# Performance work log

Measured on AMD Instinct MI355X. Metric: run time of the kernel, lower is better.

Reference implementation:

```python
import jax, jax.numpy as jnp
import numpy as np

TREE_DEPTH = 6
TEMPERATURE = 1.0


def setup_inputs() -> dict:
    key = jax.random.key(0)
    k1, k2, k3, k4, k5 = jax.random.split(key, 5)
    B, D = 8192, 512
    T = 64                      # n_trees
    N = 2 ** TREE_DEPTH - 1    # internal nodes = 63
    L = 2 ** TREE_DEPTH        # leaves = 64
    C = 100                    # classes
    return {
        "x": jax.random.normal(k1, (B, D), dtype=jnp.float32),
        "split_weights": jax.random.normal(k2, (T, N, D), dtype=jnp.float32),
        "split_bias": jax.random.normal(k3, (T, N), dtype=jnp.float32),
        "leaf_logits": jax.random.normal(k4, (T, L, C), dtype=jnp.float32),
        "tree_weights": jax.random.uniform(k5, (T,), dtype=jnp.float32),
    }


def reference(x, split_weights, split_bias, leaf_logits, tree_weights):
    # All node decisions for all trees in one batched GEMM: [B, T, N]
    dec = jax.nn.sigmoid(
        (jnp.einsum("bd,tnd->btn", x, split_weights) + split_bias) / TEMPERATURE
    )
    B = x.shape[0]
    T = split_weights.shape[0]
    L = leaf_logits.shape[1]  # 2 ** TREE_DEPTH
    leaf_ids = jnp.arange(L)
    # Cumulative product of routing probs along each leaf's root-to-leaf path.
    leaf_probs = jnp.ones((B, T, L), dtype=x.dtype)
    for d in range(TREE_DEPTH):
        # ancestor node (level order) of each leaf at this depth
        node_idx = (2 ** d - 1) + (leaf_ids >> (TREE_DEPTH - d))
        # 1 -> right child (prob = dec), 0 -> left child (prob = 1 - dec)
        bit = (leaf_ids >> (TREE_DEPTH - d - 1)) & 1
        dd = dec[:, :, node_idx]  # [B, T, L]
        leaf_probs = leaf_probs * jnp.where(bit.astype(bool), dd, 1.0 - dd)
    tree_out = jax.nn.softmax(leaf_logits, axis=-1)  # [T, L, C]
    # weighted sum over trees of (leaf_probs @ leaf class dists)
    return jnp.einsum("btl,tlc,t->bc", leaf_probs, tree_out, tree_weights)
```

## Files before the change

### kernel.cpp

```cpp
#include <hip/hip_runtime.h>

#define TREES 64
#define NN 63
#define LL 64
#define CC 100
#define CPAD 112
#define DD 512
#define BB 8192

typedef __attribute__((ext_vector_type(8))) _Float16 f16x8;
typedef __attribute__((ext_vector_type(4))) _Float16 f16x4;
typedef __attribute__((ext_vector_type(4))) float floatx4;

#define XH_WS   0
#define SWH_WS  8388608
#define W2T_WS  12582912

__device__ __forceinline__ void gl_lds16(const _Float16* g, char* lds) {
    __builtin_amdgcn_global_load_lds(
        (const __attribute__((address_space(1))) unsigned int*)g,
        (__attribute__((address_space(3))) unsigned int*)lds, 16, 0, 0);
}

__device__ __forceinline__ f16x8 cvt8(const float* s) {
    float4 a = *(const float4*)s, b = *(const float4*)(s + 4);
    f16x8 h;
    h[0]=(_Float16)a.x; h[1]=(_Float16)a.y; h[2]=(_Float16)a.z; h[3]=(_Float16)a.w;
    h[4]=(_Float16)b.x; h[5]=(_Float16)b.y; h[6]=(_Float16)b.z; h[7]=(_Float16)b.w;
    return h;
}

__device__ __forceinline__ float fsig(float x) {
    return __builtin_amdgcn_rcpf(1.f + __expf(-x));
}

__global__ __launch_bounds__(256) void prep_kernel(
    const float* __restrict__ x, const float* __restrict__ sw,
    const float* __restrict__ leaf_logits, const float* __restrict__ tree_w,
    _Float16* __restrict__ xh, _Float16* __restrict__ swh,
    _Float16* __restrict__ w2T, float* __restrict__ out)
{
    if (blockIdx.x < 3072) {
        int i = blockIdx.x * 256 + threadIdx.x;
        if (i < 524288) {
            int tile = i >> 10, cidx = i & 1023;
            int row = cidx >> 3, c = cidx & 7;
            int rb = tile >> 3, kt = tile & 7;
            int gk = kt * 64 + ((c ^ (row & 7)) << 3);
            *(f16x8*)(xh + (size_t)i * 8) = cvt8(x + (size_t)(rb * 128 + row) * DD + gk);
        } else {
            int j = i - 524288;
            if (j < 262144) {
                int tile = j >> 10, cidx = j & 1023;
                int col = cidx >> 3, c = cidx & 7;
                int cb = tile >> 3, kt = tile & 7;
                int tt = col >> 6, node = col & 63;
                f16x8 h = (f16x8)(_Float16)0.f;
                if (node < NN) {
                    int gk = kt * 64 + ((c ^ (col & 7)) << 3);
                    h = cvt8(sw + (size_t)((cb * 2 + tt) * NN + node) * DD + gk);
                }
                *(f16x8*)(swh + (size_t)j * 8) = h;
            }
        }
    } else if (blockIdx.x < 4096) {
        int row  = (blockIdx.x - 3072) * 4 + (threadIdx.x >> 6);
        int lane = threadIdx.x & 63;
        int t = row >> 6, l = row & 63;
        const float* src = leaf_logits + (size_t)row * CC;
        float v0 = (lane < CC)      ? src[lane]      : -1e30f;
        float v1 = (lane + 64 < CC) ? src[lane + 64] : -1e30f;
        float m = fmaxf(v0, v1);
#pragma unroll
        for (int off = 32; off > 0; off >>= 1)
            m = fmaxf(m, __shfl_down(m, off, 64));
        m = __shfl(m, 0, 64);
        float e0 = (lane < CC)      ? __expf(v0 - m) : 0.f;
        float e1 = (lane + 64 < CC) ? __expf(v1 - m) : 0.f;
        float s = e0 + e1;
#pragma unroll
        for (int off = 32; off > 0; off >>= 1)
            s += __shfl_down(s, off, 64);
        s = __shfl(s, 0, 64);
        float scale = tree_w[t] / s;
        _Float16* base = w2T + (size_t)t * CPAD * LL;
#define LSWZ(c) ((((l >> 3) ^ ((c) & 7)) << 3) | (l & 7))
        if (lane < CC)      base[(size_t)lane * LL + LSWZ(lane)]               = (_Float16)(e0 * scale);
        if (lane + 64 < CC) base[(size_t)(lane + 64) * LL + LSWZ(lane + 64)]   = (_Float16)(e1 * scale);
        if (lane < CPAD - CC) base[(size_t)(CC + lane) * LL + LSWZ(CC + lane)] = (_Float16)0.f;
#undef LSWZ
    } else {
        int i = (blockIdx.x - 4096) * 1024 + threadIdx.x * 4;
        *(float4*)(out + i) = make_float4(0.f, 0.f, 0.f, 0.f);
    }
}

#define SETB 24576
#define A_SMEM 49152
__global__ __launch_bounds__(256, 3) void fused_kernel(
    const _Float16* __restrict__ xh,
    const _Float16* __restrict__ swh,
    const float* __restrict__ sb,
    const _Float16* __restrict__ w2T,
    float* __restrict__ out)
{
    __shared__ __align__(16) char smem[A_SMEM];
    _Float16* dec = (_Float16*)smem;
    _Float16* lpl = (_Float16*)(smem + SETB);

    const int tid  = threadIdx.x;
    const int lane = tid & 63;
    const int wid  = tid >> 6;
    const int quad = lane >> 4;
    const int l15  = lane & 15;
    const int rb   = blockIdx.x;
    const int tc   = blockIdx.y;
    const int rb2  = rb >> 1;
    const int half = rb & 1;

    floatx4 oacc2[7];
#pragma unroll
    for (int ni = 0; ni < 7; ++ni) oacc2[ni] = (floatx4)0.f;

    const _Float16* xtile = xh + (size_t)rb2 * 65536 + (size_t)half * 4096;

#define STAGE(WT, KT, SOFF)                                                    \
    {                                                                          \
        _Pragma("unroll")                                                      \
        for (int j = 0; j < 2; ++j)                                            \
            gl_lds16(xtile + (KT) * 8192 + j * 2048 + wid * 512 + lane * 8,    \
                     smem + (SOFF) + j * 4096 + wid * 1024);                   \
        _Pragma("unroll")                                                      \
        for (int j = 0; j < 4; ++j)                                            \
            gl_lds16((WT) + (KT) * 8192 + j * 2048 + wid * 512 + lane * 8,     \
                     smem + (SOFF) + 8192 + j * 4096 + wid * 1024);            \
    }

    STAGE(swh + (size_t)(tc * 4) * 65536, 0, 0);
    __syncthreads();

    for (int tg = 0; tg < 4; ++tg) {
        const int cb = tc * 4 + tg;
        const _Float16* wtile = swh + (size_t)cb * 65536;

        float bias_v[2];
        {
            int mytree = cb * 2 + (wid >> 1);
#pragma unroll
            for (int ni = 0; ni < 2; ++ni) {
                int nd = 32 * (wid & 1) + 16 * ni + l15;
                bias_v[ni] = (nd < NN) ? sb[mytree * NN + nd] : 0.f;
            }
        }

        floatx4 acc[4][2];
#pragma unroll
        for (int i = 0; i < 4; ++i)
#pragma unroll
            for (int j = 0; j < 2; ++j) acc[i][j] = (floatx4)0.f;

        for (int kt = 0; kt < 8; ++kt) {
            if (kt < 7)
                STAGE(wtile, kt + 1, ((kt + 1) & 1) * SETB);
            const int cur = (kt & 1) * SETB;
            const _Float16* xs = (const _Float16*)(smem + cur);
            const _Float16* wl = (const _Float16*)(smem + cur + 8192);
#pragma unroll
            for (int ks = 0; ks < 2; ++ks) {
                f16x8 af[4], bf[2];
#pragma unroll
                for (int mi = 0; mi < 4; ++mi) {
                    int r = 16 * mi + l15;
                    af[mi] = *(const f16x8*)&xs[r * 64 + ((((ks << 2) | quad) ^ (r & 7)) << 3)];
                }
#pragma unroll
                for (int ni = 0; ni < 2; ++ni) {
                    int r = 32 * wid + 16 * ni + l15;
                    bf[ni] = *(const f16x8*)&wl[r * 64 + ((((ks << 2) | quad) ^ (r & 7)) << 3)];
                }
#pragma unroll
                for (int mi = 0; mi < 4; ++mi)
#pragma unroll
                    for (int ni = 0; ni < 2; ++ni)
                        acc[mi][ni] = __builtin_amdgcn_mfma_f32_16x16x32_f16(
                            af[mi], bf[ni], acc[mi][ni], 0, 0, 0);
            }
            __syncthreads();
        }

#pragma unroll
        for (int mi = 0; mi < 4; ++mi) {
            int r0 = 16 * mi + 4 * quad;
#pragma unroll
            for (int ni = 0; ni < 2; ++ni) {
                int col = 32 * wid + 16 * ni + l15;
                f16x4 v;
#pragma unroll
                for (int r = 0; r < 4; ++r)
                    v[r] = (_Float16)(acc[mi][ni][r] + bias_v[ni]);
                *(f16x4*)&dec[col * 66 + r0] = v;
            }
        }
        __syncthreads();

        const int u    = tid >> 7;
        const int tt   = (tid >> 6) & 1;
        const int lrow = tid & 63;
        const int tb   = tt * 64;
        f16x8 lpreg[4];
        {
#define SIG(n) fsig((float)dec[(tb + (n)) * 66 + lrow])
            float d0 = SIG(0);
            float p1 = u ? d0 : 1.f - d0;
            float d1 = SIG(1 + u);
#pragma unroll
            for (int b8 = 0; b8 < 4; ++b8) {
                int i4 = b8 >> 1, i3 = b8 & 1;
                float p2 = p1 * (i4 ? d1 : 1.f - d1);
                float d2 = SIG(3 + 2 * u + i4);
                float p3 = p2 * (i3 ? d2 : 1.f - d2);
                float d3 = SIG(7 + 4 * u + b8);
                f16x8 blk;
#pragma unroll
                for (int i2 = 0; i2 < 2; ++i2) {
                    float p4 = p3 * (i2 ? d3 : 1.f - d3);
                    float d4 = SIG(15 + 8 * u + 2 * b8 + i2);
#pragma unroll
                    for (int i1 = 0; i1 < 2; ++i1) {
                        float p5 = p4 * (i1 ? d4 : 1.f - d4);
                        float d5 = SIG(31 + 16 * u + 4 * b8 + 2 * i2 + i1);
                        blk[i2 * 4 + i1 * 2 + 0] = (_Float16)(p5 * (1.f - d5));
                        blk[i2 * 4 + i1 * 2 + 1] = (_Float16)(p5 * d5);
                    }
                }
                lpreg[b8] = blk;
            }
#undef SIG
        }
#pragma unroll
        for (int b8 = 0; b8 < 4; ++b8) {
            int q = u * 4 + b8;
            *(f16x8*)&lpl[tt * 4096 + lrow * 64 + ((q ^ (lrow & 7)) << 3)] = lpreg[b8];
        }
        __syncthreads();

        if (tg < 3)
            STAGE(swh + (size_t)(cb + 1) * 65536, 0, 0);

        {
            const int tree0 = cb * 2;
            const int rbase = wid * 16;
#pragma unroll
            for (int t = 0; t < 2; ++t) {
                const _Float16* bp = w2T + (size_t)(tree0 + t) * (CPAD * LL) + (size_t)l15 * 64;
                const _Float16* lplt = lpl + t * 4096;
#pragma unroll
                for (int ks = 0; ks < 2; ++ks) {
                    const int sw = (((ks << 2) | quad) ^ (l15 & 7)) << 3;
                    f16x8 bbv[7], abv;
#pragma unroll
                    for (int ni = 0; ni < 7; ++ni)
                        bbv[ni] = *(const f16x8*)(bp + ni * 16 * 64 + sw);
                    abv = *(const f16x8*)&lplt[(rbase + l15) * 64 + sw];
#pragma unroll
                    for (int ni = 0; ni < 7; ++ni)
                        oacc2[ni] = __builtin_amdgcn_mfma_f32_16x16x32_f16(
                            abv, bbv[ni], oacc2[ni], 0, 0, 0);
                }
            }
        }
        __syncthreads();
    }
#undef STAGE

    {
        const int rbase2 = rb * 64 + wid * 16 + 4 * quad;
#pragma unroll
        for (int ni = 0; ni < 7; ++ni) {
            int col = 16 * ni + l15;
            if (col < CC) {
#pragma unroll
                for (int r = 0; r < 4; ++r)
                    unsafeAtomicAdd(&out[(size_t)(rbase2 + r) * CC + col],
                                    oacc2[ni][r]);
            }
        }
    }
}

extern "C" void kernel_launch(void* const* d_in, const int* in_sizes, int n_in,
                              void* d_out, int out_size, void* d_ws, size_t ws_size,
                              hipStream_t stream) {
    const float* x  = (const float*)d_in[0];
    const float* sw = (const float*)d_in[1];
    const float* sb = (const float*)d_in[2];
    const float* ll = (const float*)d_in[3];
    const float* tw = (const float*)d_in[4];
    float* out = (float*)d_out;
    _Float16* xh  = (_Float16*)((char*)d_ws + XH_WS);
    _Float16* swh = (_Float16*)((char*)d_ws + SWH_WS);
    _Float16* w2T = (_Float16*)((char*)d_ws + W2T_WS);

    prep_kernel<<<dim3(4896), 256, 0, stream>>>(x, sw, ll, tw, xh, swh, w2T, out);
    fused_kernel<<<dim3(128, 8), 256, 0, stream>>>(xh, swh, sb, w2T, out);
}
```

Before: 179.3 us.

## Load x fragments directly from global, shrink LDS to raise occupancy

Stops staging the x tile through LDS and has each wave read its A fragments directly from global memory, keeping only the split-weight tiles double-buffered in LDS. This cuts shared memory per block from 48KB to about 33KB, which lets launch bounds move from 3 to 4 blocks per CU. The barrier placement is also reworked: one sync moves to the top of each k-step and the trailing sync per tree group is dropped. The cost is that x is re-read from global/L2 by every block and wave with no LDS reuse, and the new barrier ordering adds hazard risk between the LDS writes of dec/lpl and the staging buffers.

```diff
diff --git a/kernel.cpp b/kernel.cpp
--- a/kernel.cpp
+++ b/kernel.cpp
@@ -95,9 +95,10 @@
     }
 }
 
-#define SETB 24576
-#define A_SMEM 49152
-__global__ __launch_bounds__(256, 3) void fused_kernel(
+#define BUF1 16384
+#define LPL_OFF 16896
+#define A_SMEM 33280
+__global__ __launch_bounds__(256, 4) void fused_kernel(
     const _Float16* __restrict__ xh,
     const _Float16* __restrict__ swh,
     const float* __restrict__ sb,
@@ -106,7 +107,7 @@
 {
     __shared__ __align__(16) char smem[A_SMEM];
     _Float16* dec = (_Float16*)smem;
-    _Float16* lpl = (_Float16*)(smem + SETB);
+    _Float16* lpl = (_Float16*)(smem + LPL_OFF);
 
     const int tid  = threadIdx.x;
     const int lane = tid & 63;
@@ -124,20 +125,15 @@
 
     const _Float16* xtile = xh + (size_t)rb2 * 65536 + (size_t)half * 4096;
 
-#define STAGE(WT, KT, SOFF)                                                    \
+#define STAGE_W(WT, KT, SOFF)                                                  \
     {                                                                          \
-        _Pragma("unroll")                                                      \
-        for (int j = 0; j < 2; ++j)                                            \
-            gl_lds16(xtile + (KT) * 8192 + j * 2048 + wid * 512 + lane * 8,    \
-                     smem + (SOFF) + j * 4096 + wid * 1024);                   \
         _Pragma("unroll")                                                      \
         for (int j = 0; j < 4; ++j)                                            \
             gl_lds16((WT) + (KT) * 8192 + j * 2048 + wid * 512 + lane * 8,     \
-                     smem + (SOFF) + 8192 + j * 4096 + wid * 1024);            \
+                     smem + (SOFF) + j * 4096 + wid * 1024);                   \
     }
 
-    STAGE(swh + (size_t)(tc * 4) * 65536, 0, 0);
-    __syncthreads();
+    STAGE_W(swh + (size_t)(tc * 4) * 65536, 0, 0)
 
     for (int tg = 0; tg < 4; ++tg) {
         const int cb = tc * 4 + tg;
@@ -160,19 +156,25 @@
             for (int j = 0; j < 2; ++j) acc[i][j] = (floatx4)0.f;
 
         for (int kt = 0; kt < 8; ++kt) {
+            __syncthreads();
             if (kt < 7)
-                STAGE(wtile, kt + 1, ((kt + 1) & 1) * SETB);
-            const int cur = (kt & 1) * SETB;
-            const _Float16* xs = (const _Float16*)(smem + cur);
-            const _Float16* wl = (const _Float16*)(smem + cur + 8192);
-#pragma unroll
-            for (int ks = 0; ks < 2; ++ks) {
-                f16x8 af[4], bf[2];
+                STAGE_W(wtile, kt + 1, ((kt + 1) & 1) * BUF1)
+
+            f16x8 af[2][4];
+#pragma unroll
+            for (int ks = 0; ks < 2; ++ks)
 #pragma unroll
                 for (int mi = 0; mi < 4; ++mi) {
                     int r = 16 * mi + l15;
-                    af[mi] = *(const f16x8*)&xs[r * 64 + ((((ks << 2) | quad) ^ (r & 7)) << 3)];
-                }
+                    int kc = 4 * ks + quad;
+                    af[ks][mi] = *(const f16x8*)(xtile + kt * 8192 + r * 64
+                                                 + ((kc ^ (r & 7)) << 3));
+                }
+
+            const _Float16* wl = (const _Float16*)(smem + (kt & 1) * BUF1);
+#pragma unroll
+            for (int ks = 0; ks < 2; ++ks) {
+                f16x8 bf[2];
 #pragma unroll
                 for (int ni = 0; ni < 2; ++ni) {
                     int r = 32 * wid + 16 * ni + l15;
@@ -183,10 +185,10 @@
 #pragma unroll
                     for (int ni = 0; ni < 2; ++ni)
                         acc[mi][ni] = __builtin_amdgcn_mfma_f32_16x16x32_f16(
-                            af[mi], bf[ni], acc[mi][ni], 0, 0, 0);
-            }
-            __syncthreads();
-        }
+                            af[ks][mi], bf[ni], acc[mi][ni], 0, 0, 0);
+            }
+        }
+        __syncthreads();
 
 #pragma unroll
         for (int mi = 0; mi < 4; ++mi) {
@@ -245,7 +247,7 @@
         __syncthreads();
 
         if (tg < 3)
-            STAGE(swh + (size_t)(cb + 1) * 65536, 0, 0);
+            STAGE_W(swh + (size_t)(cb + 1) * 65536, 0, 0)
 
         {
             const int tree0 = cb * 2;
@@ -269,9 +271,8 @@
                 }
             }
         }
-        __syncthreads();
     }
-#undef STAGE
+#undef STAGE_W
 
     {
         const int rbase2 = rb * 64 + wid * 16 + 4 * quad;
```

Result: slower. 394.3 us (+119.9%).
